# Optimization experiments

Measured on AMD Instinct MI355X. Metric: run time of the kernel, lower is better.

Reference implementation:

```python
import jax, jax.numpy as jnp
import numpy as np

B, T, F, H = 131072, 5, 30, 20


def setup_inputs() -> dict:
    key = jax.random.key(0)
    ks = jax.random.split(key, 13)
    inp = {"x": jax.random.normal(ks[0], (B, T, F), dtype=jnp.float32)}
    names_w = ["wf", "wi", "wo", "wc"]
    names_u = ["uf", "ui", "uo", "uc"]
    names_b = ["bf", "bi", "bo", "bc"]
    for j, n in enumerate(names_w):
        inp[n] = jax.random.normal(ks[1 + j], (F, H), dtype=jnp.float32) * 0.1
    for j, n in enumerate(names_u):
        inp[n] = jax.random.normal(ks[5 + j], (H, H), dtype=jnp.float32) * 0.1
    for j, n in enumerate(names_b):
        inp[n] = jax.random.normal(ks[9 + j], (1, H), dtype=jnp.float32) * 0.1
    return inp


def reference(x, wf, wi, wo, wc, uf, ui, uo, uc, bf, bi, bo, bc):
    # Note: at t=0 the original skips the recurrent term and uses ct = it*cht;
    # that is exactly equivalent to scanning with h0 = c0 = 0.
    b = x.shape[0]
    h = wf.shape[1]
    # Precompute the input-side gate projections for all timesteps in one GEMM
    # per gate: [B,T,F] @ [F,H] -> [B,T,H]. Same math, fewer launches.
    gx_f = jnp.einsum("btf,fh->bth", x, wf) + bf
    gx_i = jnp.einsum("btf,fh->bth", x, wi) + bi
    gx_o = jnp.einsum("btf,fh->bth", x, wo) + bo
    gx_c = jnp.einsum("btf,fh->bth", x, wc) + bc
    # time-major for scan: [T,B,H]
    gx = jnp.stack([gx_f.transpose(1, 0, 2), gx_i.transpose(1, 0, 2),
                    gx_o.transpose(1, 0, 2), gx_c.transpose(1, 0, 2)], axis=1)

    def step(carry, g):
        ht, ct = carry
        gf, gi, go, gc = g[0], g[1], g[2], g[3]
        ft = jax.nn.sigmoid(gf + ht @ uf)
        it = jax.nn.sigmoid(gi + ht @ ui)
        ot = jax.nn.sigmoid(go + ht @ uo)
        cht = jnp.tanh(gc + ht @ uc)
        ct = ft * ct + it * cht
        ht = ot * jnp.tanh(ct)
        return (ht, ct), ht

    h0 = jnp.zeros((b, h), dtype=x.dtype)
    c0 = jnp.zeros((b, h), dtype=x.dtype)
    _, hs = jax.lax.scan(step, (h0, c0), gx)  # hs: [T,B,H]
    return hs.transpose(1, 0, 2)  # return_sequences=True -> [B,T,H]
```

## Files before the change

### kernel.cpp

```cpp
#include <hip/hip_runtime.h>
#include <hip/hip_bf16.h>

namespace {

constexpr int T = 5, F = 30, H = 20;
constexpr int BATCH = 131072;
constexpr int BPB = 64;
constexpr int XRS = 20;
constexpr int HRS = 132;

typedef __attribute__((ext_vector_type(8))) short bf16x8;
typedef __attribute__((ext_vector_type(4))) float f32x4;

union Frag16 { uint2 d2[2]; uint4 d4; unsigned u32[4]; bf16x8 v; };
union Pack2 { __hip_bfloat162 h2; unsigned u; };

__device__ __forceinline__ float sig(float v) {
  return __builtin_amdgcn_rcpf(1.0f + __builtin_amdgcn_exp2f(v * -1.44269504f));
}
__device__ __forceinline__ float tanh_s(float v) {
  return fmaf(2.0f,
              __builtin_amdgcn_rcpf(1.0f + __builtin_amdgcn_exp2f(v * -2.88539008f)),
              -1.0f);
}
__device__ __forceinline__ unsigned short f2bf(float f) {
  unsigned u = __float_as_uint(f);
  return (unsigned short)((u + 0x7FFFu + ((u >> 16) & 1u)) >> 16);
}

__global__ void lstm_pack(
    const float* __restrict__ wf, const float* __restrict__ wi,
    const float* __restrict__ wo, const float* __restrict__ wc,
    const float* __restrict__ uf, const float* __restrict__ ui,
    const float* __restrict__ uo, const float* __restrict__ uc,
    const float* __restrict__ bf, const float* __restrict__ bi,
    const float* __restrict__ bo, const float* __restrict__ bc,
    bf16x8* __restrict__ ws)
{
  const int i = blockIdx.x * 256 + threadIdx.x;
  if (i >= 640) return;
  const int lane = i & 63, sel = (i >> 6) & 1, m = i >> 7;
  const int r15 = lane & 15, q = lane >> 4;
  const int gA = r15 & 3, jA = r15 >> 2;
  const int jj = 4 * m + jA;

  const float* Wg = (gA == 0) ? wf : (gA == 1) ? wi : (gA == 2) ? wo : wc;
  const float* Ug = (gA == 0) ? uf : (gA == 1) ? ui : (gA == 2) ? uo : uc;
  const float* Bg = (gA == 0) ? bf : (gA == 1) ? bi : (gA == 2) ? bo : bc;

  Frag16 fr;
#pragma unroll
  for (int e = 0; e < 4; ++e) {
    const int k0 = 8 * q + 2 * e, k1 = k0 + 1;
    float v0, v1;
    if (sel == 0) {
      v0 = (k0 < F) ? Wg[k0 * H + jj] : (k0 == F ? Bg[jj] : 0.f);
      v1 = (k1 < F) ? Wg[k1 * H + jj] : 0.f;
    } else {
      v0 = (k0 < H) ? Ug[k0 * H + jj] : 0.f;
      v1 = (k1 < H) ? Ug[k1 * H + jj] : 0.f;
    }
    Pack2 p; p.h2 = __float22bfloat162_rn(float2{v0, v1});
    fr.u32[e] = p.u;
  }
  ws[(m * 2 + sel) * 64 + lane] = fr.v;
}

__global__ __launch_bounds__(256, 4) void lstm_main(
    const float* __restrict__ x,
    const bf16x8* __restrict__ wsfrag,
    float* __restrict__ out)
{
  const int tid  = threadIdx.x;
  const int lane = tid & 63;
  const int wv   = tid >> 6;
  const int r15  = lane & 15;
  const int q    = lane >> 4;
  const int b0   = blockIdx.x * BPB;
  const int w0   = 16 * wv;

  const float* xwave = x + (size_t)(b0 + w0) * (T * F);
  float*       owave = out + (size_t)(b0 + w0) * (T * H);

  __shared__ __align__(16) unsigned xsb[BPB * XRS];
  __shared__ __align__(16) unsigned short hist[BPB * HRS];

  bf16x8 wfrag[5], ufrag[5];
#pragma unroll
  for (int m = 0; m < 5; ++m) {
    wfrag[m] = wsfrag[(m * 2 + 0) * 64 + lane];
    ufrag[m] = wsfrag[(m * 2 + 1) * 64 + lane];
  }

  if (tid < BPB) xsb[tid * XRS + 15] = 0x00003F80u;

#pragma unroll
  for (int j = 0; j < 4; ++j) {
    int s = lane + 64 * j;
    int r = s >> 4, cs = s & 15;
    if (cs < 15) {
      float2 v = *(const float2*)(xwave + r * (T * F) + 2 * cs);
      Pack2 p; p.h2 = __float22bfloat162_rn(v);
      xsb[(w0 + r) * XRS + cs] = p.u;
    }
  }

  float cst[5];
#pragma unroll
  for (int m = 0; m < 5; ++m) cst[m] = 0.f;
  float2 pf2[4];

#pragma unroll
  for (int t = 0; t < T; ++t) {
    Frag16 fx;
    fx.d4 = *(const uint4*)&xsb[(w0 + r15) * XRS + 4 * q];

    if (t + 1 < T) {
#pragma unroll
      for (int j = 0; j < 4; ++j) {
        int s = lane + 64 * j;
        int r = s >> 4, cs = s & 15;
        if (cs < 15)
          pf2[j] = *(const float2*)(xwave + r * (T * F) + (t + 1) * F + 2 * cs);
      }
    }

    f32x4 acc[5];
#pragma unroll
    for (int m = 0; m < 5; ++m)
      acc[m] = __builtin_amdgcn_mfma_f32_16x16x32_bf16(
          wfrag[m], fx.v, f32x4{0.f, 0.f, 0.f, 0.f}, 0, 0, 0);

    if (t > 0) {
      Frag16 fh;
      const unsigned short* hp = &hist[(w0 + r15) * HRS + 24 * (t - 1) + 8 * q];
      fh.d2[0] = *(const uint2*)(hp);
      fh.d2[1] = *(const uint2*)(hp + 4);
#pragma unroll
      for (int m = 0; m < 5; ++m)
        acc[m] = __builtin_amdgcn_mfma_f32_16x16x32_bf16(
            ufrag[m], fh.v, acc[m], 0, 0, 0);
    }

#pragma unroll
    for (int m = 0; m < 5; ++m) {
      float fg = sig(acc[m][0]);
      float ig = sig(acc[m][1]);
      float og = sig(acc[m][2]);
      float ch = tanh_s(acc[m][3]);
      float cn = fmaf(fg, cst[m], ig * ch);
      cst[m] = cn;
      float hn = og * tanh_s(cn);
      hist[(w0 + r15) * HRS + 24 * t + 4 * m + q] = f2bf(hn);
    }

    if (t + 1 < T) {
#pragma unroll
      for (int j = 0; j < 4; ++j) {
        int s = lane + 64 * j;
        int r = s >> 4, cs = s & 15;
        if (cs < 15) {
          Pack2 p; p.h2 = __float22bfloat162_rn(pf2[j]);
          xsb[(w0 + r) * XRS + cs] = p.u;
        }
      }
    }
  }

#pragma unroll
  for (int k = 0; k < 7; ++k) {
    unsigned g = lane + 64 * k;
    if (g < 400) {
      unsigned r = g / 25u, c4 = 4 * (g % 25u);
      unsigned tb = c4 / 20u, j0 = c4 % 20u;
      uint2 pv = *(const uint2*)&hist[(w0 + r) * HRS + 24 * tb + j0];
      float4 v;
      v.x = __uint_as_float(pv.x << 16);
      v.y = __uint_as_float(pv.x & 0xFFFF0000u);
      v.z = __uint_as_float(pv.y << 16);
      v.w = __uint_as_float(pv.y & 0xFFFF0000u);
      *(float4*)(owave + 4 * g) = v;
    }
  }
}

}

extern "C" void kernel_launch(void* const* d_in, const int* in_sizes, int n_in,
                              void* d_out, int out_size, void* d_ws, size_t ws_size,
                              hipStream_t stream) {
  const float* x  = (const float*)d_in[0];
  const float* wf = (const float*)d_in[1];
  const float* wi = (const float*)d_in[2];
  const float* wo = (const float*)d_in[3];
  const float* wc = (const float*)d_in[4];
  const float* uf = (const float*)d_in[5];
  const float* ui = (const float*)d_in[6];
  const float* uo = (const float*)d_in[7];
  const float* uc = (const float*)d_in[8];
  const float* bf = (const float*)d_in[9];
  const float* bi = (const float*)d_in[10];
  const float* bo = (const float*)d_in[11];
  const float* bc = (const float*)d_in[12];
  float* out = (float*)d_out;
  bf16x8* ws = (bf16x8*)d_ws;

  hipLaunchKernelGGL(lstm_pack, dim3(3), dim3(256), 0, stream,
                     wf, wi, wo, wc, uf, ui, uo, uc, bf, bi, bo, bc, ws);
  hipLaunchKernelGGL(lstm_main, dim3(BATCH / BPB), dim3(256), 0, stream,
                     x, ws, out);
}
```

Before: 39.84 us.

## Keep recurrent state in registers via permuted U fragment layout, load x directly

```diff
diff --git a/kernel.cpp b/kernel.cpp
--- a/kernel.cpp
+++ b/kernel.cpp
@@ -6,13 +6,12 @@
 constexpr int T = 5, F = 30, H = 20;
 constexpr int BATCH = 131072;
 constexpr int BPB = 64;
-constexpr int XRS = 20;
-constexpr int HRS = 132;
+constexpr int HRS = 120;
 
 typedef __attribute__((ext_vector_type(8))) short bf16x8;
 typedef __attribute__((ext_vector_type(4))) float f32x4;
 
-union Frag16 { uint2 d2[2]; uint4 d4; unsigned u32[4]; bf16x8 v; };
+union Frag16 { unsigned u32[4]; bf16x8 v; };
 union Pack2 { __hip_bfloat162 h2; unsigned u; };
 
 __device__ __forceinline__ float sig(float v) {
@@ -22,10 +21,6 @@
   return fmaf(2.0f,
               __builtin_amdgcn_rcpf(1.0f + __builtin_amdgcn_exp2f(v * -2.88539008f)),
               -1.0f);
-}
-__device__ __forceinline__ unsigned short f2bf(float f) {
-  unsigned u = __float_as_uint(f);
-  return (unsigned short)((u + 0x7FFFu + ((u >> 16) & 1u)) >> 16);
 }
 
 __global__ void lstm_pack(
@@ -51,14 +46,15 @@
   Frag16 fr;
 #pragma unroll
   for (int e = 0; e < 4; ++e) {
-    const int k0 = 8 * q + 2 * e, k1 = k0 + 1;
     float v0, v1;
     if (sel == 0) {
+      const int k0 = 8 * q + 2 * e, k1 = k0 + 1;
       v0 = (k0 < F) ? Wg[k0 * H + jj] : (k0 == F ? Bg[jj] : 0.f);
       v1 = (k1 < F) ? Wg[k1 * H + jj] : 0.f;
     } else {
-      v0 = (k0 < H) ? Ug[k0 * H + jj] : 0.f;
-      v1 = (k1 < H) ? Ug[k1 * H + jj] : 0.f;
+      const int i0 = 2 * e, i1 = 2 * e + 1;
+      v0 = (i0 < 5) ? Ug[(4 * i0 + q) * H + jj] : 0.f;
+      v1 = (i1 < 5) ? Ug[(4 * i1 + q) * H + jj] : 0.f;
     }
     Pack2 p; p.h2 = __float22bfloat162_rn(float2{v0, v1});
     fr.u32[e] = p.u;
@@ -66,7 +62,7 @@
   ws[(m * 2 + sel) * 64 + lane] = fr.v;
 }
 
-__global__ __launch_bounds__(256, 4) void lstm_main(
+__global__ __launch_bounds__(256, 3) void lstm_main(
     const float* __restrict__ x,
     const bf16x8* __restrict__ wsfrag,
     float* __restrict__ out)
@@ -79,10 +75,9 @@
   const int b0   = blockIdx.x * BPB;
   const int w0   = 16 * wv;
 
-  const float* xwave = x + (size_t)(b0 + w0) * (T * F);
+  const float* xrow = x + (size_t)(b0 + w0 + r15) * (T * F);
   float*       owave = out + (size_t)(b0 + w0) * (T * H);
 
-  __shared__ __align__(16) unsigned xsb[BPB * XRS];
   __shared__ __align__(16) unsigned short hist[BPB * HRS];
 
   bf16x8 wfrag[5], ufrag[5];
@@ -92,37 +87,46 @@
     ufrag[m] = wsfrag[(m * 2 + 1) * 64 + lane];
   }
 
-  if (tid < BPB) xsb[tid * XRS + 15] = 0x00003F80u;
-
-#pragma unroll
-  for (int j = 0; j < 4; ++j) {
-    int s = lane + 64 * j;
-    int r = s >> 4, cs = s & 15;
-    if (cs < 15) {
-      float2 v = *(const float2*)(xwave + r * (T * F) + 2 * cs);
-      Pack2 p; p.h2 = __float22bfloat162_rn(v);
-      xsb[(w0 + r) * XRS + cs] = p.u;
-    }
+  const int xo0 = 8 * q, xo1 = 8 * q + 2, xo2 = 8 * q + 4;
+  const int xo3 = (q == 3) ? (8 * q + 4) : (8 * q + 6);
+
+  float2 xbuf[2][4];
+#pragma unroll
+  for (int j = 0; j < 1; ++j) {
+    xbuf[0][0] = *(const float2*)(xrow + xo0);
+    xbuf[0][1] = *(const float2*)(xrow + xo1);
+    xbuf[0][2] = *(const float2*)(xrow + xo2);
+    xbuf[0][3] = *(const float2*)(xrow + xo3);
   }
 
   float cst[5];
 #pragma unroll
   for (int m = 0; m < 5; ++m) cst[m] = 0.f;
-  float2 pf2[4];
+
+  unsigned pd[T][3];
+  unsigned ph0 = 0, ph1 = 0, ph2 = 0;
 
 #pragma unroll
   for (int t = 0; t < T; ++t) {
+    if (t + 1 < T) {
+      const float* xp = xrow + (t + 1) * F;
+      xbuf[(t + 1) & 1][0] = *(const float2*)(xp + xo0);
+      xbuf[(t + 1) & 1][1] = *(const float2*)(xp + xo1);
+      xbuf[(t + 1) & 1][2] = *(const float2*)(xp + xo2);
+      xbuf[(t + 1) & 1][3] = *(const float2*)(xp + xo3);
+    }
+
     Frag16 fx;
-    fx.d4 = *(const uint4*)&xsb[(w0 + r15) * XRS + 4 * q];
-
-    if (t + 1 < T) {
-#pragma unroll
-      for (int j = 0; j < 4; ++j) {
-        int s = lane + 64 * j;
-        int r = s >> 4, cs = s & 15;
-        if (cs < 15)
-          pf2[j] = *(const float2*)(xwave + r * (T * F) + (t + 1) * F + 2 * cs);
-      }
+    {
+      Pack2 p0, p1, p2, p3;
+      p0.h2 = __float22bfloat162_rn(xbuf[t & 1][0]);
+      p1.h2 = __float22bfloat162_rn(xbuf[t & 1][1]);
+      p2.h2 = __float22bfloat162_rn(xbuf[t & 1][2]);
+      p3.h2 = __float22bfloat162_rn(xbuf[t & 1][3]);
+      fx.u32[0] = p0.u;
+      fx.u32[1] = p1.u;
+      fx.u32[2] = (q == 3) ? p3.u : p2.u;
+      fx.u32[3] = (q == 3) ? 0x00003F80u : p3.u;
     }
 
     f32x4 acc[5];
@@ -133,15 +137,17 @@
 
     if (t > 0) {
       Frag16 fh;
-      const unsigned short* hp = &hist[(w0 + r15) * HRS + 24 * (t - 1) + 8 * q];
-      fh.d2[0] = *(const uint2*)(hp);
-      fh.d2[1] = *(const uint2*)(hp + 4);
+      fh.u32[0] = ph0;
+      fh.u32[1] = ph1;
+      fh.u32[2] = ph2;
+      fh.u32[3] = 0u;
 #pragma unroll
       for (int m = 0; m < 5; ++m)
         acc[m] = __builtin_amdgcn_mfma_f32_16x16x32_bf16(
             ufrag[m], fh.v, acc[m], 0, 0, 0);
     }
 
+    float hn[5];
 #pragma unroll
     for (int m = 0; m < 5; ++m) {
       float fg = sig(acc[m][0]);
@@ -150,23 +156,29 @@
       float ch = tanh_s(acc[m][3]);
       float cn = fmaf(fg, cst[m], ig * ch);
       cst[m] = cn;
-      float hn = og * tanh_s(cn);
-      hist[(w0 + r15) * HRS + 24 * t + 4 * m + q] = f2bf(hn);
-    }
-
-    if (t + 1 < T) {
-#pragma unroll
-      for (int j = 0; j < 4; ++j) {
-        int s = lane + 64 * j;
-        int r = s >> 4, cs = s & 15;
-        if (cs < 15) {
-          Pack2 p; p.h2 = __float22bfloat162_rn(pf2[j]);
-          xsb[(w0 + r) * XRS + cs] = p.u;
-        }
-      }
-    }
-  }
-
+      hn[m] = og * tanh_s(cn);
+    }
+    {
+      Pack2 a, b, c;
+      a.h2 = __float22bfloat162_rn(float2{hn[0], hn[1]});
+      b.h2 = __float22bfloat162_rn(float2{hn[2], hn[3]});
+      c.h2 = __float22bfloat162_rn(float2{hn[4], 0.f});
+      ph0 = a.u; ph1 = b.u; ph2 = c.u;
+      pd[t][0] = a.u; pd[t][1] = b.u; pd[t][2] = c.u;
+    }
+  }
+
+  {
+    unsigned short* hrow = hist + (w0 + r15) * HRS;
+#pragma unroll
+    for (int t = 0; t < T; ++t) {
+      hrow[24 * t +  0 + q] = (unsigned short)(pd[t][0]);
+      hrow[24 * t +  4 + q] = (unsigned short)(pd[t][0] >> 16);
+      hrow[24 * t +  8 + q] = (unsigned short)(pd[t][1]);
+      hrow[24 * t + 12 + q] = (unsigned short)(pd[t][1] >> 16);
+      hrow[24 * t + 16 + q] = (unsigned short)(pd[t][2]);
+    }
+  }
 #pragma unroll
   for (int k = 0; k < 7; ++k) {
     unsigned g = lane + 64 * k;
```

Result: faster. 38.68 us (-2.9%).
